# Kernel optimization log

Hardware: AMD Instinct MI355X
Metric: run time of the kernel (lower is better)

## Reference

```python
import jax, jax.numpy as jnp
import numpy as np

N_TOKENS = 262144
NUM_CODES = 512
CODE_DIM = 64


def setup_inputs() -> dict:
    key = jax.random.key(0)
    k1, k2 = jax.random.split(key)
    z_e = jax.random.normal(k1, (N_TOKENS, CODE_DIM), dtype=jnp.float32)
    embeddings = jax.random.normal(k2, (NUM_CODES, CODE_DIM), dtype=jnp.float32)
    return {"z_e": z_e, "embeddings": embeddings}


def reference(z_e, embeddings):
    # distances[n, k] = ||z_e[n] - e_k||^2, expanded matmul form as in the torch code
    # (N, K) = (N, 1) - 2 * (N, D) @ (D, K) + (K,)
    distances = (
        jnp.sum(z_e ** 2, axis=1, keepdims=True)
        - 2.0 * (z_e @ embeddings.T)
        + jnp.sum(embeddings ** 2, axis=1)
    )
    indices = jnp.argmin(distances, axis=1)          # (N,)
    z_q = embeddings[indices]                        # (N, D) gather
    # straight-through: identity gradient to z_e, none through the gather
    z_q_st = z_e + jax.lax.stop_gradient(z_q - z_e)
    commitment_loss = jnp.mean((jax.lax.stop_gradient(z_e) - z_q) ** 2)
    return z_q_st, indices, commitment_loss
```

## Files before the change

### kernel.cpp

```cpp
#include <hip/hip_runtime.h>


typedef short  bf16x8 __attribute__((ext_vector_type(8)));
typedef float  f32x4  __attribute__((ext_vector_type(4)));

static constexpr int N_TOK = 262144;
static constexpr int K     = 512;
static constexpr int D     = 64;
static constexpr float THRESH = 0.01f;
static constexpr int NBLK_A = N_TOK / 1024;

static constexpr size_t WS_ESQ   = 0;
static constexpr size_t WS_BL    = 2048;
static constexpr size_t WS_EFRAG = 10240;

#define GLDS16(G, L) __builtin_amdgcn_global_load_lds(                    \
    (const __attribute__((address_space(1))) void*)(G),                   \
    (__attribute__((address_space(3))) void*)(L), 16, 0, 0)

__global__ __launch_bounds__(512) void prep_kernel(
    const float* __restrict__ emb, unsigned short* __restrict__ ef,
    float* __restrict__ esq) {
  int idx  = blockIdx.x * 512 + threadIdx.x;
  int code = idx >> 6, d = idx & 63;
  float s  = -2.0f * emb[code * 64 + d];
  unsigned u  = __float_as_uint(s);
  unsigned hi = (u + 0x7FFFu + ((u >> 16) & 1u)) >> 16;
  float lof   = s - __uint_as_float(hi << 16);
  unsigned v2 = __float_as_uint(lof);
  unsigned lo = (v2 + 0x7FFFu + ((v2 >> 16) & 1u)) >> 16;
  int tile = code >> 4, row = code & 15;
  int c = (d >> 5) & 1, g = (d >> 3) & 3, i = d & 7;
  int lane = row + (g << 4);
  size_t base = ((size_t)tile * 256 + (size_t)c * 128) * 8;
  ef[base + (size_t)(0 * 64 + lane) * 8 + i] = (unsigned short)hi;
  ef[base + (size_t)(1 * 64 + lane) * 8 + i] = (unsigned short)lo;
  if (threadIdx.x < 8) {
    int k = blockIdx.x * 8 + threadIdx.x;
    const float4* row4 = reinterpret_cast<const float4*>(emb + (size_t)k * D);
    float acc = 0.f;
#pragma unroll
    for (int j = 0; j < 16; ++j) {
      float4 v = row4[j];
      acc = fmaf(v.x, v.x, acc); acc = fmaf(v.y, v.y, acc);
      acc = fmaf(v.z, v.z, acc); acc = fmaf(v.w, v.w, acc);
    }
    esq[k] = acc;
  }
}

__device__ __forceinline__ void split8(float4 a, float4 b,
                                       bf16x8& h, bf16x8& lo) {
  float v[8] = {a.x, a.y, a.z, a.w, b.x, b.y, b.z, b.w};
#pragma unroll
  for (int i = 0; i < 8; ++i) {
    unsigned u  = __float_as_uint(v[i]);
    unsigned hi = (u + 0x7FFFu + ((u >> 16) & 1u)) >> 16;
    float lof   = v[i] - __uint_as_float(hi << 16);
    unsigned v2 = __float_as_uint(lof);
    unsigned l2 = (v2 + 0x7FFFu + ((v2 >> 16) & 1u)) >> 16;
    h[i]  = (short)hi;
    lo[i] = (short)l2;
  }
}

#define ARGMIN4(C, BASE, BEST, SECOND, BIDXV)               \
  {                                                         \
    _Pragma("unroll")                                       \
    for (int r = 0; r < 4; ++r) {                           \
      float v = (C)[r];                                     \
      bool lt = v < (BEST);                                 \
      float mn = fminf((SECOND), v);                        \
      (SECOND) = lt ? (BEST) : mn;                          \
      (BIDXV)  = lt ? ((BASE) + r) : (BIDXV);               \
      (BEST)   = lt ? v : (BEST);                           \
    }                                                       \
  }

__global__ __launch_bounds__(1024) void vq_mfma(
    const float* __restrict__ z_e, const float* __restrict__ emb,
    const unsigned short* __restrict__ efrag, const float* __restrict__ esq_g,
    float* __restrict__ out_zq, float* __restrict__ out_idx,
    float* __restrict__ block_loss) {
  __shared__ float esql[K];
  __shared__ __align__(16) short lds_e[65536];
  __shared__ int   sIdx[512];
  __shared__ float wsm[16];

  const int t  = threadIdx.x;
  const int l  = t & 63;
  const int wu = __builtin_amdgcn_readfirstlane(t >> 6);
  const int g  = l >> 4, g4 = g << 2;
  const int blk0 = blockIdx.x * 1024;

  if (t < K) esql[t] = esq_g[t];

  const bf16x8* EF = reinterpret_cast<const bf16x8*>(efrag);
#pragma unroll
  for (int r = 0; r < 8; ++r)
    GLDS16(EF + r * 1024 + t, &lds_e[r * 8192 + wu * 512]);
  asm volatile("s_waitcnt vmcnt(0)" ::: "memory");
  __builtin_amdgcn_s_barrier();

  float blsum = 0.f;

  for (int pass = 0; pass < 2; ++pass) {
    const int tok0 = blk0 + pass * 512 + wu * 32;

    bf16x8 zh0A, zl0A, zh1A, zl1A, zh0B, zl0B, zh1B, zl1B;
    {
      const int rowA = tok0 + (l & 15);
      const float* zp = z_e + (size_t)rowA * D + g * 8;
      float4 q0 = *reinterpret_cast<const float4*>(zp);
      float4 q1 = *reinterpret_cast<const float4*>(zp + 4);
      float4 q2 = *reinterpret_cast<const float4*>(zp + 32);
      float4 q3 = *reinterpret_cast<const float4*>(zp + 36);
      split8(q0, q1, zh0A, zl0A);
      split8(q2, q3, zh1A, zl1A);
      zp += (size_t)16 * D;
      q0 = *reinterpret_cast<const float4*>(zp);
      q1 = *reinterpret_cast<const float4*>(zp + 4);
      q2 = *reinterpret_cast<const float4*>(zp + 32);
      q3 = *reinterpret_cast<const float4*>(zp + 36);
      split8(q0, q1, zh0B, zl0B);
      split8(q2, q3, zh1B, zl1B);
    }

    float bestA = 3.402823466e38f, secondA = 3.402823466e38f;
    float bestB = 3.402823466e38f, secondB = 3.402823466e38f;
    int idxA = 0, idxB = 0;

    for (int tile = 0; tile < 32; ++tile) {
      const bf16x8* tb =
          reinterpret_cast<const bf16x8*>(&lds_e[(size_t)tile * 2048]);
      f32x4 CA = *reinterpret_cast<const f32x4*>(&esql[tile * 16 + g4]);
      f32x4 CB = CA;
      bf16x8 e0h = tb[l], e0l = tb[64 + l];
      bf16x8 e1h = tb[128 + l], e1l = tb[192 + l];
      __builtin_amdgcn_s_setprio(1);
      CA = __builtin_amdgcn_mfma_f32_16x16x32_bf16(e0h, zh0A, CA, 0, 0, 0);
      CB = __builtin_amdgcn_mfma_f32_16x16x32_bf16(e0h, zh0B, CB, 0, 0, 0);
      CA = __builtin_amdgcn_mfma_f32_16x16x32_bf16(e0h, zl0A, CA, 0, 0, 0);
      CB = __builtin_amdgcn_mfma_f32_16x16x32_bf16(e0h, zl0B, CB, 0, 0, 0);
      CA = __builtin_amdgcn_mfma_f32_16x16x32_bf16(e0l, zh0A, CA, 0, 0, 0);
      CB = __builtin_amdgcn_mfma_f32_16x16x32_bf16(e0l, zh0B, CB, 0, 0, 0);
      CA = __builtin_amdgcn_mfma_f32_16x16x32_bf16(e1h, zh1A, CA, 0, 0, 0);
      CB = __builtin_amdgcn_mfma_f32_16x16x32_bf16(e1h, zh1B, CB, 0, 0, 0);
      CA = __builtin_amdgcn_mfma_f32_16x16x32_bf16(e1h, zl1A, CA, 0, 0, 0);
      CB = __builtin_amdgcn_mfma_f32_16x16x32_bf16(e1h, zl1B, CB, 0, 0, 0);
      CA = __builtin_amdgcn_mfma_f32_16x16x32_bf16(e1l, zh1A, CA, 0, 0, 0);
      CB = __builtin_amdgcn_mfma_f32_16x16x32_bf16(e1l, zh1B, CB, 0, 0, 0);
      __builtin_amdgcn_s_setprio(0);

      const int base = tile * 16 + g4;
      ARGMIN4(CA, base, bestA, secondA, idxA)
      ARGMIN4(CB, base, bestB, secondB, idxB)
    }

#pragma unroll
    for (int mask = 16; mask <= 32; mask <<= 1) {
      float ob, os; int oi; bool take; float hi2;
      ob = __shfl_xor(bestA, mask); oi = __shfl_xor(idxA, mask);
      os = __shfl_xor(secondA, mask);
      hi2 = fmaxf(bestA, ob);
      secondA = fminf(secondA, fminf(os, hi2));
      take = (ob < bestA) || (ob == bestA && oi < idxA);
      bestA = take ? ob : bestA; idxA = take ? oi : idxA;

      ob = __shfl_xor(bestB, mask); oi = __shfl_xor(idxB, mask);
      os = __shfl_xor(secondB, mask);
      hi2 = fmaxf(bestB, ob);
      secondB = fminf(secondB, fminf(os, hi2));
      take = (ob < bestB) || (ob == bestB && oi < idxB);
      bestB = take ? ob : bestB; idxB = take ? oi : idxB;
    }

    if (l < 16) {
      sIdx[wu * 32 + l]      = idxA;
      sIdx[wu * 32 + 16 + l] = idxB;
    }

    {
      bool fA = (l < 16) && ((secondA - bestA) < THRESH);
      bool fB = (l < 16) && ((secondB - bestB) < THRESH);
      unsigned long long ba = __ballot(fA);
      unsigned long long bb = __ballot(fB);
      unsigned mask = (unsigned)((ba & 0xFFFFull) | ((bb & 0xFFFFull) << 16));
      while (mask) {
        const int j = __builtin_ctz(mask);
        mask &= mask - 1;
        const int n = tok0 + j;
        const float4* zr =
            reinterpret_cast<const float4*>(z_e + (size_t)n * D);
        float best = 3.402823466e38f; int bid = 0;
#pragma unroll 1
        for (int half2 = 0; half2 < 2; ++half2) {
          float acc[4];
#pragma unroll
          for (int m = 0; m < 4; ++m) acc[m] = 0.f;
#pragma unroll 1
          for (int i = 0; i < 16; ++i) {
            float4 z4 = zr[i];
#pragma unroll
            for (int m = 0; m < 4; ++m) {
              const float4 e4 = *reinterpret_cast<const float4*>(
                  emb + (size_t)(l + 64 * (half2 * 4 + m)) * D + 4 * i);
              acc[m] = fmaf(z4.x, e4.x, acc[m]);
              acc[m] = fmaf(z4.y, e4.y, acc[m]);
              acc[m] = fmaf(z4.z, e4.z, acc[m]);
              acc[m] = fmaf(z4.w, e4.w, acc[m]);
            }
          }
#pragma unroll
          for (int m = 0; m < 4; ++m) {
            const int code = l + 64 * (half2 * 4 + m);
            float s = fmaf(-2.f, acc[m], esq_g[code]);
            if (s < best) { best = s; bid = code; }
          }
        }
#pragma unroll
        for (int mk = 1; mk <= 32; mk <<= 1) {
          float ob = __shfl_xor(best, mk);
          int   oi = __shfl_xor(bid, mk);
          bool take = (ob < best) || (ob == best && oi < bid);
          best = take ? ob : best;
          bid  = take ? oi : bid;
        }
        if (l == 0) sIdx[wu * 32 + j] = bid;
      }
    }

    {
      const int tk = l >> 1, h = l & 1;
      const int n = tok0 + tk;
      const int bi = sIdx[wu * 32 + tk];
      const float4* er =
          reinterpret_cast<const float4*>(emb + (size_t)bi * D);
      const float4* zr =
          reinterpret_cast<const float4*>(z_e + (size_t)n * D);
      float4* orow = reinterpret_cast<float4*>(out_zq + (size_t)n * D);
      float lsum = 0.f;
#pragma unroll
      for (int j = 0; j < 8; ++j) {
        int i = h * 8 + j;
        float4 Q = er[i], Z = zr[i];
        float dx = Q.x - Z.x, dy = Q.y - Z.y, dz = Q.z - Z.z, dw = Q.w - Z.w;
        float4 st;
        st.x = Z.x + dx; st.y = Z.y + dy; st.z = Z.z + dz; st.w = Z.w + dw;
        orow[i] = st;
        lsum = fmaf(dx, dx, lsum); lsum = fmaf(dy, dy, lsum);
        lsum = fmaf(dz, dz, lsum); lsum = fmaf(dw, dw, lsum);
      }
      if (h == 0) out_idx[n] = (float)bi;
      float s = lsum;
#pragma unroll
      for (int off = 32; off > 0; off >>= 1) s += __shfl_xor(s, off, 64);
      blsum += s;
    }
  }

  if (l == 0) wsm[wu] = blsum;
  __syncthreads();
  if (t == 0) {
    float s = 0.f;
#pragma unroll
    for (int i = 0; i < 16; ++i) s += wsm[i];
    block_loss[blockIdx.x] = s;
  }
}

__global__ __launch_bounds__(256) void loss_finalize(
    const float* __restrict__ bl, float* __restrict__ out_loss) {
  __shared__ float sm[256];
  const int t = threadIdx.x;
  sm[t] = bl[t];
  __syncthreads();
#pragma unroll
  for (int off = 128; off > 0; off >>= 1) {
    if (t < off) sm[t] += sm[t + off];
    __syncthreads();
  }
  if (t == 0) out_loss[0] = sm[0] * (1.0f / 16777216.0f);
}

extern "C" void kernel_launch(void* const* d_in, const int* in_sizes, int n_in,
                              void* d_out, int out_size, void* d_ws, size_t ws_size,
                              hipStream_t stream) {
  const float* z_e = (const float*)d_in[0];
  const float* emb = (const float*)d_in[1];

  float* out      = (float*)d_out;
  float* out_zq   = out;
  float* out_idx  = out + (size_t)N_TOK * D;
  float* out_loss = out_idx + N_TOK;

  char* wsb = (char*)d_ws;
  float*          esqp = (float*)(wsb + WS_ESQ);
  float*          bl   = (float*)(wsb + WS_BL);
  unsigned short* ef   = (unsigned short*)(wsb + WS_EFRAG);

  prep_kernel<<<64, 512, 0, stream>>>(emb, ef, esqp);
  vq_mfma<<<NBLK_A, 1024, 0, stream>>>(z_e, emb, ef, esqp, out_zq, out_idx, bl);
  loss_finalize<<<1, 256, 0, stream>>>(bl, out_loss);
}
```

Baseline: 104.0 us.

## Process 64 tokens per wave in one pass, overlapping z loads with LDS fill

Replaces the two-pass loop (32 tokens per wave per pass) with a single pass where each wave handles 64 tokens as four 16-row MFMA fragments. Each LDS codebook fragment load now feeds four MFMAs instead of two, and the z_e fragment loads are issued before the wait on the codebook LDS fill so the two overlap. The epilogue gives each lane one token row instead of pairing two lanes per row. This doubles accumulator and fragment register pressure, which may lower occupancy or cause spills, and the per-lane row stores are less coalesced.

Result: slower. 112.2 us (+7.8%).

```diff
diff --git a/kernel.cpp b/kernel.cpp
--- a/kernel.cpp
+++ b/kernel.cpp
@@ -77,6 +77,16 @@
     }                                                       \
   }
 
+#define ZFRAG(ZP, H0, L0, H1, L1)                                          \
+  {                                                                        \
+    float4 q0 = *reinterpret_cast<const float4*>(ZP);                      \
+    float4 q1 = *reinterpret_cast<const float4*>((ZP) + 4);                \
+    float4 q2 = *reinterpret_cast<const float4*>((ZP) + 32);               \
+    float4 q3 = *reinterpret_cast<const float4*>((ZP) + 36);               \
+    split8(q0, q1, H0, L0);                                                \
+    split8(q2, q3, H1, L1);                                                \
+  }
+
 __global__ __launch_bounds__(1024) void vq_mfma(
     const float* __restrict__ z_e, const float* __restrict__ emb,
     const unsigned short* __restrict__ efrag, const float* __restrict__ esq_g,
@@ -84,14 +94,14 @@
     float* __restrict__ block_loss) {
   __shared__ float esql[K];
   __shared__ __align__(16) short lds_e[65536];
-  __shared__ int   sIdx[512];
+  __shared__ int   sIdx[1024];
   __shared__ float wsm[16];
 
   const int t  = threadIdx.x;
   const int l  = t & 63;
   const int wu = __builtin_amdgcn_readfirstlane(t >> 6);
   const int g  = l >> 4, g4 = g << 2;
-  const int blk0 = blockIdx.x * 1024;
+  const int tok0 = blockIdx.x * 1024 + wu * 64;
 
   if (t < K) esql[t] = esq_g[t];
 
@@ -99,167 +109,175 @@
 #pragma unroll
   for (int r = 0; r < 8; ++r)
     GLDS16(EF + r * 1024 + t, &lds_e[r * 8192 + wu * 512]);
+
+  bf16x8 zh0A, zl0A, zh1A, zl1A, zh0B, zl0B, zh1B, zl1B;
+  bf16x8 zh0C, zl0C, zh1C, zl1C, zh0D, zl0D, zh1D, zl1D;
+  {
+    const float* zp = z_e + (size_t)(tok0 + (l & 15)) * D + g * 8;
+    ZFRAG(zp, zh0A, zl0A, zh1A, zl1A)
+    zp += (size_t)16 * D;
+    ZFRAG(zp, zh0B, zl0B, zh1B, zl1B)
+    zp += (size_t)16 * D;
+    ZFRAG(zp, zh0C, zl0C, zh1C, zl1C)
+    zp += (size_t)16 * D;
+    ZFRAG(zp, zh0D, zl0D, zh1D, zl1D)
+  }
+
   asm volatile("s_waitcnt vmcnt(0)" ::: "memory");
   __builtin_amdgcn_s_barrier();
 
-  float blsum = 0.f;
-
-  for (int pass = 0; pass < 2; ++pass) {
-    const int tok0 = blk0 + pass * 512 + wu * 32;
-
-    bf16x8 zh0A, zl0A, zh1A, zl1A, zh0B, zl0B, zh1B, zl1B;
+  float bestA = 3.402823466e38f, secondA = 3.402823466e38f;
+  float bestB = 3.402823466e38f, secondB = 3.402823466e38f;
+  float bestC = 3.402823466e38f, secondC = 3.402823466e38f;
+  float bestD = 3.402823466e38f, secondD = 3.402823466e38f;
+  int idxA = 0, idxB = 0, idxC = 0, idxD = 0;
+
+  for (int tile = 0; tile < 32; ++tile) {
+    const bf16x8* tb =
+        reinterpret_cast<const bf16x8*>(&lds_e[(size_t)tile * 2048]);
+    f32x4 CA = *reinterpret_cast<const f32x4*>(&esql[tile * 16 + g4]);
+    f32x4 CB = CA, CC = CA, CD = CA;
     {
-      const int rowA = tok0 + (l & 15);
-      const float* zp = z_e + (size_t)rowA * D + g * 8;
-      float4 q0 = *reinterpret_cast<const float4*>(zp);
-      float4 q1 = *reinterpret_cast<const float4*>(zp + 4);
-      float4 q2 = *reinterpret_cast<const float4*>(zp + 32);
-      float4 q3 = *reinterpret_cast<const float4*>(zp + 36);
-      split8(q0, q1, zh0A, zl0A);
-      split8(q2, q3, zh1A, zl1A);
-      zp += (size_t)16 * D;
-      q0 = *reinterpret_cast<const float4*>(zp);
-      q1 = *reinterpret_cast<const float4*>(zp + 4);
-      q2 = *reinterpret_cast<const float4*>(zp + 32);
-      q3 = *reinterpret_cast<const float4*>(zp + 36);
-      split8(q0, q1, zh0B, zl0B);
-      split8(q2, q3, zh1B, zl1B);
-    }
-
-    float bestA = 3.402823466e38f, secondA = 3.402823466e38f;
-    float bestB = 3.402823466e38f, secondB = 3.402823466e38f;
-    int idxA = 0, idxB = 0;
-
-    for (int tile = 0; tile < 32; ++tile) {
-      const bf16x8* tb =
-          reinterpret_cast<const bf16x8*>(&lds_e[(size_t)tile * 2048]);
-      f32x4 CA = *reinterpret_cast<const f32x4*>(&esql[tile * 16 + g4]);
-      f32x4 CB = CA;
       bf16x8 e0h = tb[l], e0l = tb[64 + l];
-      bf16x8 e1h = tb[128 + l], e1l = tb[192 + l];
       __builtin_amdgcn_s_setprio(1);
       CA = __builtin_amdgcn_mfma_f32_16x16x32_bf16(e0h, zh0A, CA, 0, 0, 0);
       CB = __builtin_amdgcn_mfma_f32_16x16x32_bf16(e0h, zh0B, CB, 0, 0, 0);
+      CC = __builtin_amdgcn_mfma_f32_16x16x32_bf16(e0h, zh0C, CC, 0, 0, 0);
+      CD = __builtin_amdgcn_mfma_f32_16x16x32_bf16(e0h, zh0D, CD, 0, 0, 0);
       CA = __builtin_amdgcn_mfma_f32_16x16x32_bf16(e0h, zl0A, CA, 0, 0, 0);
       CB = __builtin_amdgcn_mfma_f32_16x16x32_bf16(e0h, zl0B, CB, 0, 0, 0);
+      CC = __builtin_amdgcn_mfma_f32_16x16x32_bf16(e0h, zl0C, CC, 0, 0, 0);
+      CD = __builtin_amdgcn_mfma_f32_16x16x32_bf16(e0h, zl0D, CD, 0, 0, 0);
       CA = __builtin_amdgcn_mfma_f32_16x16x32_bf16(e0l, zh0A, CA, 0, 0, 0);
       CB = __builtin_amdgcn_mfma_f32_16x16x32_bf16(e0l, zh0B, CB, 0, 0, 0);
+      CC = __builtin_amdgcn_mfma_f32_16x16x32_bf16(e0l, zh0C, CC, 0, 0, 0);
+      CD = __builtin_amdgcn_mfma_f32_16x16x32_bf16(e0l, zh0D, CD, 0, 0, 0);
+      __builtin_amdgcn_s_setprio(0);
+    }
+    {
+      bf16x8 e1h = tb[128 + l], e1l = tb[192 + l];
+      __builtin_amdgcn_s_setprio(1);
       CA = __builtin_amdgcn_mfma_f32_16x16x32_bf16(e1h, zh1A, CA, 0, 0, 0);
       CB = __builtin_amdgcn_mfma_f32_16x16x32_bf16(e1h, zh1B, CB, 0, 0, 0);
+      CC = __builtin_amdgcn_mfma_f32_16x16x32_bf16(e1h, zh1C, CC, 0, 0, 0);
+      CD = __builtin_amdgcn_mfma_f32_16x16x32_bf16(e1h, zh1D, CD, 0, 0, 0);
       CA = __builtin_amdgcn_mfma_f32_16x16x32_bf16(e1h, zl1A, CA, 0, 0, 0);
       CB = __builtin_amdgcn_mfma_f32_16x16x32_bf16(e1h, zl1B, CB, 0, 0, 0);
+      CC = __builtin_amdgcn_mfma_f32_16x16x32_bf16(e1h, zl1C, CC, 0, 0, 0);
+      CD = __builtin_amdgcn_mfma_f32_16x16x32_bf16(e1h, zl1D, CD, 0, 0, 0);
       CA = __builtin_amdgcn_mfma_f32_16x16x32_bf16(e1l, zh1A, CA, 0, 0, 0);
       CB = __builtin_amdgcn_mfma_f32_16x16x32_bf16(e1l, zh1B, CB, 0, 0, 0);
+      CC = __builtin_amdgcn_mfma_f32_16x16x32_bf16(e1l, zh1C, CC, 0, 0, 0);
+      CD = __builtin_amdgcn_mfma_f32_16x16x32_bf16(e1l, zh1D, CD, 0, 0, 0);
       __builtin_amdgcn_s_setprio(0);
-
-      const int base = tile * 16 + g4;
-      ARGMIN4(CA, base, bestA, secondA, idxA)
-      ARGMIN4(CB, base, bestB, secondB, idxB)
-    }
-
-#pragma unroll
-    for (int mask = 16; mask <= 32; mask <<= 1) {
-      float ob, os; int oi; bool take; float hi2;
-      ob = __shfl_xor(bestA, mask); oi = __shfl_xor(idxA, mask);
-      os = __shfl_xor(secondA, mask);
-      hi2 = fmaxf(bestA, ob);
-      secondA = fminf(secondA, fminf(os, hi2));
-      take = (ob < bestA) || (ob == bestA && oi < idxA);
-      bestA = take ? ob : bestA; idxA = take ? oi : idxA;
-
-      ob = __shfl_xor(bestB, mask); oi = __shfl_xor(idxB, mask);
-      os = __shfl_xor(secondB, mask);
-      hi2 = fmaxf(bestB, ob);
-      secondB = fminf(secondB, fminf(os, hi2));
-      take = (ob < bestB) || (ob == bestB && oi < idxB);
-      bestB = take ? ob : bestB; idxB = take ? oi : idxB;
-    }
-
-    if (l < 16) {
-      sIdx[wu * 32 + l]      = idxA;
-      sIdx[wu * 32 + 16 + l] = idxB;
-    }
-
-    {
-      bool fA = (l < 16) && ((secondA - bestA) < THRESH);
-      bool fB = (l < 16) && ((secondB - bestB) < THRESH);
-      unsigned long long ba = __ballot(fA);
-      unsigned long long bb = __ballot(fB);
-      unsigned mask = (unsigned)((ba & 0xFFFFull) | ((bb & 0xFFFFull) << 16));
-      while (mask) {
-        const int j = __builtin_ctz(mask);
-        mask &= mask - 1;
-        const int n = tok0 + j;
-        const float4* zr =
-            reinterpret_cast<const float4*>(z_e + (size_t)n * D);
-        float best = 3.402823466e38f; int bid = 0;
+    }
+
+    const int base = tile * 16 + g4;
+    ARGMIN4(CA, base, bestA, secondA, idxA)
+    ARGMIN4(CB, base, bestB, secondB, idxB)
+    ARGMIN4(CC, base, bestC, secondC, idxC)
+    ARGMIN4(CD, base, bestD, secondD, idxD)
+  }
+
+#pragma unroll
+  for (int mask = 16; mask <= 32; mask <<= 1) {
+    float ob, os; int oi; bool take; float hi2;
+#define RED(BEST, SECOND, IDX)                                  \
+    ob = __shfl_xor(BEST, mask); oi = __shfl_xor(IDX, mask);    \
+    os = __shfl_xor(SECOND, mask);                              \
+    hi2 = fmaxf(BEST, ob);                                      \
+    SECOND = fminf(SECOND, fminf(os, hi2));                     \
+    take = (ob < BEST) || (ob == BEST && oi < IDX);             \
+    BEST = take ? ob : BEST; IDX = take ? oi : IDX;
+    RED(bestA, secondA, idxA)
+    RED(bestB, secondB, idxB)
+    RED(bestC, secondC, idxC)
+    RED(bestD, secondD, idxD)
+#undef RED
+  }
+
+  if (l < 16) {
+    sIdx[wu * 64 + l]      = idxA;
+    sIdx[wu * 64 + 16 + l] = idxB;
+    sIdx[wu * 64 + 32 + l] = idxC;
+    sIdx[wu * 64 + 48 + l] = idxD;
+  }
+
+  {
+    bool fA = (l < 16) && ((secondA - bestA) < THRESH);
+    bool fB = (l < 16) && ((secondB - bestB) < THRESH);
+    bool fC = (l < 16) && ((secondC - bestC) < THRESH);
+    bool fD = (l < 16) && ((secondD - bestD) < THRESH);
+    unsigned long long m =  (__ballot(fA) & 0xFFFFull)
+                         | ((__ballot(fB) & 0xFFFFull) << 16)
+                         | ((__ballot(fC) & 0xFFFFull) << 32)
+                         | ((__ballot(fD) & 0xFFFFull) << 48);
+    while (m) {
+      const int j = __builtin_ctzll(m);
+      m &= m - 1;
+      const int n = tok0 + j;
+      const float4* zr = reinterpret_cast<const float4*>(z_e + (size_t)n * D);
+      float best = 3.402823466e38f; int bid = 0;
 #pragma unroll 1
-        for (int half2 = 0; half2 < 2; ++half2) {
-          float acc[4];
-#pragma unroll
-          for (int m = 0; m < 4; ++m) acc[m] = 0.f;
+      for (int half2 = 0; half2 < 2; ++half2) {
+        float acc[4];
+#pragma unroll
+        for (int mm = 0; mm < 4; ++mm) acc[mm] = 0.f;
 #pragma unroll 1
-          for (int i = 0; i < 16; ++i) {
-            float4 z4 = zr[i];
-#pragma unroll
-            for (int m = 0; m < 4; ++m) {
-              const float4 e4 = *reinterpret_cast<const float4*>(
-                  emb + (size_t)(l + 64 * (half2 * 4 + m)) * D + 4 * i);
-              acc[m] = fmaf(z4.x, e4.x, acc[m]);
-              acc[m] = fmaf(z4.y, e4.y, acc[m]);
-              acc[m] = fmaf(z4.z, e4.z, acc[m]);
-              acc[m] = fmaf(z4.w, e4.w, acc[m]);
-            }
-          }
-#pragma unroll
-          for (int m = 0; m < 4; ++m) {
-            const int code = l + 64 * (half2 * 4 + m);
-            float s = fmaf(-2.f, acc[m], esq_g[code]);
-            if (s < best) { best = s; bid = code; }
+        for (int i = 0; i < 16; ++i) {
+          float4 z4 = zr[i];
+#pragma unroll
+          for (int mm = 0; mm < 4; ++mm) {
+            const float4 e4 = *reinterpret_cast<const float4*>(
+                emb + (size_t)(l + 64 * (half2 * 4 + mm)) * D + 4 * i);
+            acc[mm] = fmaf(z4.x, e4.x, acc[mm]);
+            acc[mm] = fmaf(z4.y, e4.y, acc[mm]);
+            acc[mm] = fmaf(z4.z, e4.z, acc[mm]);
+            acc[mm] = fmaf(z4.w, e4.w, acc[mm]);
           }
         }
 #pragma unroll
-        for (int mk = 1; mk <= 32; mk <<= 1) {
-          float ob = __shfl_xor(best, mk);
-          int   oi = __shfl_xor(bid, mk);
-          bool take = (ob < best) || (ob == best && oi < bid);
-          best = take ? ob : best;
-          bid  = take ? oi : bid;
+        for (int mm = 0; mm < 4; ++mm) {
+          const int code = l + 64 * (half2 * 4 + mm);
+          float s = fmaf(-2.f, acc[mm], esq_g[code]);
+          if (s < best) { best = s; bid = code; }
         }
-        if (l == 0) sIdx[wu * 32 + j] = bid;
       }
-    }
-
-    {
-      const int tk = l >> 1, h = l & 1;
-      const int n = tok0 + tk;
-      const int bi = sIdx[wu * 32 + tk];
-      const float4* er =
-          reinterpret_cast<const float4*>(emb + (size_t)bi * D);
-      const float4* zr =
-          reinterpret_cast<const float4*>(z_e + (size_t)n * D);
-      float4* orow = reinterpret_cast<float4*>(out_zq + (size_t)n * D);
-      float lsum = 0.f;
-#pragma unroll
-      for (int j = 0; j < 8; ++j) {
-        int i = h * 8 + j;
-        float4 Q = er[i], Z = zr[i];
-        float dx = Q.x - Z.x, dy = Q.y - Z.y, dz = Q.z - Z.z, dw = Q.w - Z.w;
-        float4 st;
-        st.x = Z.x + dx; st.y = Z.y + dy; st.z = Z.z + dz; st.w = Z.w + dw;
-        orow[i] = st;
-        lsum = fmaf(dx, dx, lsum); lsum = fmaf(dy, dy, lsum);
-        lsum = fmaf(dz, dz, lsum); lsum = fmaf(dw, dw, lsum);
+#pragma unroll
+      for (int mk = 1; mk <= 32; mk <<= 1) {
+        float ob = __shfl_xor(best, mk);
+        int   oi = __shfl_xor(bid, mk);
+        bool take = (ob < best) || (ob == best && oi < bid);
+        best = take ? ob : best;
+        bid  = take ? oi : bid;
       }
-      if (h == 0) out_idx[n] = (float)bi;
-      float s = lsum;
-#pragma unroll
-      for (int off = 32; off > 0; off >>= 1) s += __shfl_xor(s, off, 64);
-      blsum += s;
-    }
-  }
-
-  if (l == 0) wsm[wu] = blsum;
+      if (l == 0) sIdx[wu * 64 + j] = bid;
+    }
+  }
+
+  {
+    const int n = tok0 + l;
+    const int bi = sIdx[wu * 64 + l];
+    const float4* er = reinterpret_cast<const float4*>(emb + (size_t)bi * D);
+    const float4* zr = reinterpret_cast<const float4*>(z_e + (size_t)n * D);
+    float4* orow = reinterpret_cast<float4*>(out_zq + (size_t)n * D);
+    float lsum = 0.f;
+#pragma unroll 4
+    for (int i = 0; i < 16; ++i) {
+      float4 Q = er[i], Z = zr[i];
+      float dx = Q.x - Z.x, dy = Q.y - Z.y, dz = Q.z - Z.z, dw = Q.w - Z.w;
+      float4 st;
+      st.x = Z.x + dx; st.y = Z.y + dy; st.z = Z.z + dz; st.w = Z.w + dw;
+      orow[i] = st;
+      lsum = fmaf(dx, dx, lsum); lsum = fmaf(dy, dy, lsum);
+      lsum = fmaf(dz, dz, lsum); lsum = fmaf(dw, dw, lsum);
+    }
+    out_idx[n] = (float)bi;
+    float s = lsum;
+#pragma unroll
+    for (int off = 32; off > 0; off >>= 1) s += __shfl_xor(s, off, 64);
+    if (l == 0) wsm[wu] = s;
+  }
   __syncthreads();
   if (t == 0) {
     float s = 0.f;
```

## Stage only high-half codebook in LDS, read low half from global, one pass per block

Applied to the files above, without the earlier changes.

Halves the number of tokens per block (512 instead of 1024) so the grid doubles to 512 blocks, removing the two-pass loop. Only the high bf16 half of the codebook fragments is staged in LDS (64KB instead of 128KB), and the low half is read directly from global memory (L2/L1-cached) inside the tile loop. The z_e loads are issued before the LDS-staging wait so they overlap. The aim is lower LDS footprint and higher occupancy or more blocks per CU, at the cost of more codebook staging overall and global loads inside the hot MFMA loop. The loss finalize now sums 512 partials.

New measurement: 128.5 us. +23.6%, slower.

```diff
diff --git a/kernel.cpp b/kernel.cpp
--- a/kernel.cpp
+++ b/kernel.cpp
@@ -8,7 +8,7 @@
 static constexpr int K     = 512;
 static constexpr int D     = 64;
 static constexpr float THRESH = 0.01f;
-static constexpr int NBLK_A = N_TOK / 1024;
+static constexpr int NBLK_A = N_TOK / 512;
 
 static constexpr size_t WS_ESQ   = 0;
 static constexpr size_t WS_BL    = 2048;
@@ -83,7 +83,7 @@
     float* __restrict__ out_zq, float* __restrict__ out_idx,
     float* __restrict__ block_loss) {
   __shared__ float esql[K];
-  __shared__ __align__(16) short lds_e[65536];
+  __shared__ __align__(16) short lds_eh[32768];
   __shared__ int   sIdx[512];
   __shared__ float wsm[16];
 
@@ -91,175 +91,172 @@
   const int l  = t & 63;
   const int wu = __builtin_amdgcn_readfirstlane(t >> 6);
   const int g  = l >> 4, g4 = g << 2;
-  const int blk0 = blockIdx.x * 1024;
+  const int tok0 = blockIdx.x * 512 + wu * 32;
 
   if (t < K) esql[t] = esq_g[t];
 
   const bf16x8* EF = reinterpret_cast<const bf16x8*>(efrag);
 #pragma unroll
-  for (int r = 0; r < 8; ++r)
-    GLDS16(EF + r * 1024 + t, &lds_e[r * 8192 + wu * 512]);
+  for (int r = 0; r < 4; ++r) {
+    const int fh = r * 16 + wu;
+    const int tile = fh >> 1, c = fh & 1;
+    GLDS16(EF + (size_t)tile * 256 + c * 128 + l,
+           &lds_eh[r * 8192 + wu * 512]);
+  }
+
+  bf16x8 zh0A, zl0A, zh1A, zl1A, zh0B, zl0B, zh1B, zl1B;
+  {
+    const int rowA = tok0 + (l & 15);
+    const float* zp = z_e + (size_t)rowA * D + g * 8;
+    float4 q0 = *reinterpret_cast<const float4*>(zp);
+    float4 q1 = *reinterpret_cast<const float4*>(zp + 4);
+    float4 q2 = *reinterpret_cast<const float4*>(zp + 32);
+    float4 q3 = *reinterpret_cast<const float4*>(zp + 36);
+    split8(q0, q1, zh0A, zl0A);
+    split8(q2, q3, zh1A, zl1A);
+    zp += (size_t)16 * D;
+    q0 = *reinterpret_cast<const float4*>(zp);
+    q1 = *reinterpret_cast<const float4*>(zp + 4);
+    q2 = *reinterpret_cast<const float4*>(zp + 32);
+    q3 = *reinterpret_cast<const float4*>(zp + 36);
+    split8(q0, q1, zh0B, zl0B);
+    split8(q2, q3, zh1B, zl1B);
+  }
+
   asm volatile("s_waitcnt vmcnt(0)" ::: "memory");
   __builtin_amdgcn_s_barrier();
 
-  float blsum = 0.f;
-
-  for (int pass = 0; pass < 2; ++pass) {
-    const int tok0 = blk0 + pass * 512 + wu * 32;
-
-    bf16x8 zh0A, zl0A, zh1A, zl1A, zh0B, zl0B, zh1B, zl1B;
-    {
-      const int rowA = tok0 + (l & 15);
-      const float* zp = z_e + (size_t)rowA * D + g * 8;
-      float4 q0 = *reinterpret_cast<const float4*>(zp);
-      float4 q1 = *reinterpret_cast<const float4*>(zp + 4);
-      float4 q2 = *reinterpret_cast<const float4*>(zp + 32);
-      float4 q3 = *reinterpret_cast<const float4*>(zp + 36);
-      split8(q0, q1, zh0A, zl0A);
-      split8(q2, q3, zh1A, zl1A);
-      zp += (size_t)16 * D;
-      q0 = *reinterpret_cast<const float4*>(zp);
-      q1 = *reinterpret_cast<const float4*>(zp + 4);
-      q2 = *reinterpret_cast<const float4*>(zp + 32);
-      q3 = *reinterpret_cast<const float4*>(zp + 36);
-      split8(q0, q1, zh0B, zl0B);
-      split8(q2, q3, zh1B, zl1B);
-    }
-
-    float bestA = 3.402823466e38f, secondA = 3.402823466e38f;
-    float bestB = 3.402823466e38f, secondB = 3.402823466e38f;
-    int idxA = 0, idxB = 0;
-
-    for (int tile = 0; tile < 32; ++tile) {
-      const bf16x8* tb =
-          reinterpret_cast<const bf16x8*>(&lds_e[(size_t)tile * 2048]);
-      f32x4 CA = *reinterpret_cast<const f32x4*>(&esql[tile * 16 + g4]);
-      f32x4 CB = CA;
-      bf16x8 e0h = tb[l], e0l = tb[64 + l];
-      bf16x8 e1h = tb[128 + l], e1l = tb[192 + l];
-      __builtin_amdgcn_s_setprio(1);
-      CA = __builtin_amdgcn_mfma_f32_16x16x32_bf16(e0h, zh0A, CA, 0, 0, 0);
-      CB = __builtin_amdgcn_mfma_f32_16x16x32_bf16(e0h, zh0B, CB, 0, 0, 0);
-      CA = __builtin_amdgcn_mfma_f32_16x16x32_bf16(e0h, zl0A, CA, 0, 0, 0);
-      CB = __builtin_amdgcn_mfma_f32_16x16x32_bf16(e0h, zl0B, CB, 0, 0, 0);
-      CA = __builtin_amdgcn_mfma_f32_16x16x32_bf16(e0l, zh0A, CA, 0, 0, 0);
-      CB = __builtin_amdgcn_mfma_f32_16x16x32_bf16(e0l, zh0B, CB, 0, 0, 0);
-      CA = __builtin_amdgcn_mfma_f32_16x16x32_bf16(e1h, zh1A, CA, 0, 0, 0);
-      CB = __builtin_amdgcn_mfma_f32_16x16x32_bf16(e1h, zh1B, CB, 0, 0, 0);
-      CA = __builtin_amdgcn_mfma_f32_16x16x32_bf16(e1h, zl1A, CA, 0, 0, 0);
-      CB = __builtin_amdgcn_mfma_f32_16x16x32_bf16(e1h, zl1B, CB, 0, 0, 0);
-      CA = __builtin_amdgcn_mfma_f32_16x16x32_bf16(e1l, zh1A, CA, 0, 0, 0);
-      CB = __builtin_amdgcn_mfma_f32_16x16x32_bf16(e1l, zh1B, CB, 0, 0, 0);
-      __builtin_amdgcn_s_setprio(0);
-
-      const int base = tile * 16 + g4;
-      ARGMIN4(CA, base, bestA, secondA, idxA)
-      ARGMIN4(CB, base, bestB, secondB, idxB)
-    }
-
-#pragma unroll
-    for (int mask = 16; mask <= 32; mask <<= 1) {
-      float ob, os; int oi; bool take; float hi2;
-      ob = __shfl_xor(bestA, mask); oi = __shfl_xor(idxA, mask);
-      os = __shfl_xor(secondA, mask);
-      hi2 = fmaxf(bestA, ob);
-      secondA = fminf(secondA, fminf(os, hi2));
-      take = (ob < bestA) || (ob == bestA && oi < idxA);
-      bestA = take ? ob : bestA; idxA = take ? oi : idxA;
-
-      ob = __shfl_xor(bestB, mask); oi = __shfl_xor(idxB, mask);
-      os = __shfl_xor(secondB, mask);
-      hi2 = fmaxf(bestB, ob);
-      secondB = fminf(secondB, fminf(os, hi2));
-      take = (ob < bestB) || (ob == bestB && oi < idxB);
-      bestB = take ? ob : bestB; idxB = take ? oi : idxB;
-    }
-
-    if (l < 16) {
-      sIdx[wu * 32 + l]      = idxA;
-      sIdx[wu * 32 + 16 + l] = idxB;
-    }
-
-    {
-      bool fA = (l < 16) && ((secondA - bestA) < THRESH);
-      bool fB = (l < 16) && ((secondB - bestB) < THRESH);
-      unsigned long long ba = __ballot(fA);
-      unsigned long long bb = __ballot(fB);
-      unsigned mask = (unsigned)((ba & 0xFFFFull) | ((bb & 0xFFFFull) << 16));
-      while (mask) {
-        const int j = __builtin_ctz(mask);
-        mask &= mask - 1;
-        const int n = tok0 + j;
-        const float4* zr =
-            reinterpret_cast<const float4*>(z_e + (size_t)n * D);
-        float best = 3.402823466e38f; int bid = 0;
+  float bestA = 3.402823466e38f, secondA = 3.402823466e38f;
+  float bestB = 3.402823466e38f, secondB = 3.402823466e38f;
+  int idxA = 0, idxB = 0;
+
+  for (int tile = 0; tile < 32; ++tile) {
+    const bf16x8* loP = EF + (size_t)tile * 256 + 64 + l;
+    bf16x8 e0l = loP[0];
+    bf16x8 e1l = loP[128];
+    const bf16x8* tbh =
+        reinterpret_cast<const bf16x8*>(&lds_eh[(size_t)tile * 1024]);
+    bf16x8 e0h = tbh[l], e1h = tbh[64 + l];
+
+    f32x4 CA = *reinterpret_cast<const f32x4*>(&esql[tile * 16 + g4]);
+    f32x4 CB = CA;
+    __builtin_amdgcn_s_setprio(1);
+    CA = __builtin_amdgcn_mfma_f32_16x16x32_bf16(e0h, zh0A, CA, 0, 0, 0);
+    CB = __builtin_amdgcn_mfma_f32_16x16x32_bf16(e0h, zh0B, CB, 0, 0, 0);
+    CA = __builtin_amdgcn_mfma_f32_16x16x32_bf16(e0h, zl0A, CA, 0, 0, 0);
+    CB = __builtin_amdgcn_mfma_f32_16x16x32_bf16(e0h, zl0B, CB, 0, 0, 0);
+    CA = __builtin_amdgcn_mfma_f32_16x16x32_bf16(e0l, zh0A, CA, 0, 0, 0);
+    CB = __builtin_amdgcn_mfma_f32_16x16x32_bf16(e0l, zh0B, CB, 0, 0, 0);
+    CA = __builtin_amdgcn_mfma_f32_16x16x32_bf16(e1h, zh1A, CA, 0, 0, 0);
+    CB = __builtin_amdgcn_mfma_f32_16x16x32_bf16(e1h, zh1B, CB, 0, 0, 0);
+    CA = __builtin_amdgcn_mfma_f32_16x16x32_bf16(e1h, zl1A, CA, 0, 0, 0);
+    CB = __builtin_amdgcn_mfma_f32_16x16x32_bf16(e1h, zl1B, CB, 0, 0, 0);
+    CA = __builtin_amdgcn_mfma_f32_16x16x32_bf16(e1l, zh1A, CA, 0, 0, 0);
+    CB = __builtin_amdgcn_mfma_f32_16x16x32_bf16(e1l, zh1B, CB, 0, 0, 0);
+    __builtin_amdgcn_s_setprio(0);
+
+    const int base = tile * 16 + g4;
+    ARGMIN4(CA, base, bestA, secondA, idxA)
+    ARGMIN4(CB, base, bestB, secondB, idxB)
+  }
+
+#pragma unroll
+  for (int mask = 16; mask <= 32; mask <<= 1) {
+    float ob, os; int oi; bool take; float hi2;
+    ob = __shfl_xor(bestA, mask); oi = __shfl_xor(idxA, mask);
+    os = __shfl_xor(secondA, mask);
+    hi2 = fmaxf(bestA, ob);
+    secondA = fminf(secondA, fminf(os, hi2));
+    take = (ob < bestA) || (ob == bestA && oi < idxA);
+    bestA = take ? ob : bestA; idxA = take ? oi : idxA;
+
+    ob = __shfl_xor(bestB, mask); oi = __shfl_xor(idxB, mask);
+    os = __shfl_xor(secondB, mask);
+    hi2 = fmaxf(bestB, ob);
+    secondB = fminf(secondB, fminf(os, hi2));
+    take = (ob < bestB) || (ob == bestB && oi < idxB);
+    bestB = take ? ob : bestB; idxB = take ? oi : idxB;
+  }
+
+  if (l < 16) {
+    sIdx[wu * 32 + l]      = idxA;
+    sIdx[wu * 32 + 16 + l] = idxB;
+  }
+
+  {
+    bool fA = (l < 16) && ((secondA - bestA) < THRESH);
+    bool fB = (l < 16) && ((secondB - bestB) < THRESH);
+    unsigned long long ba = __ballot(fA);
+    unsigned long long bb = __ballot(fB);
+    unsigned mask = (unsigned)((ba & 0xFFFFull) | ((bb & 0xFFFFull) << 16));
+    while (mask) {
+      const int j = __builtin_ctz(mask);
+      mask &= mask - 1;
+      const int n = tok0 + j;
+      const float4* zr = reinterpret_cast<const float4*>(z_e + (size_t)n * D);
+      float best = 3.402823466e38f; int bid = 0;
 #pragma unroll 1
-        for (int half2 = 0; half2 < 2; ++half2) {
-          float acc[4];
-#pragma unroll
-          for (int m = 0; m < 4; ++m) acc[m] = 0.f;
+      for (int half2 = 0; half2 < 2; ++half2) {
+        float acc[4];
+#pragma unroll
+        for (int m = 0; m < 4; ++m) acc[m] = 0.f;
 #pragma unroll 1
-          for (int i = 0; i < 16; ++i) {
-            float4 z4 = zr[i];
-#pragma unroll
-            for (int m = 0; m < 4; ++m) {
-              const float4 e4 = *reinterpret_cast<const float4*>(
-                  emb + (size_t)(l + 64 * (half2 * 4 + m)) * D + 4 * i);
-              acc[m] = fmaf(z4.x, e4.x, acc[m]);
-              acc[m] = fmaf(z4.y, e4.y, acc[m]);
-              acc[m] = fmaf(z4.z, e4.z, acc[m]);
-              acc[m] = fmaf(z4.w, e4.w, acc[m]);
-            }
-          }
+        for (int i = 0; i < 16; ++i) {
+          float4 z4 = zr[i];
 #pragma unroll
           for (int m = 0; m < 4; ++m) {
-            const int code = l + 64 * (half2 * 4 + m);
-            float s = fmaf(-2.f, acc[m], esq_g[code]);
-            if (s < best) { best = s; bid = code; }
+            const float4 e4 = *reinterpret_cast<const float4*>(
+                emb + (size_t)(l + 64 * (half2 * 4 + m)) * D + 4 * i);
+            acc[m] = fmaf(z4.x, e4.x, acc[m]);
+            acc[m] = fmaf(z4.y, e4.y, acc[m]);
+            acc[m] = fmaf(z4.z, e4.z, acc[m]);
+            acc[m] = fmaf(z4.w, e4.w, acc[m]);
           }
         }
 #pragma unroll
-        for (int mk = 1; mk <= 32; mk <<= 1) {
-          float ob = __shfl_xor(best, mk);
-          int   oi = __shfl_xor(bid, mk);
-          bool take = (ob < best) || (ob == best && oi < bid);
-          best = take ? ob : best;
-          bid  = take ? oi : bid;
+        for (int m = 0; m < 4; ++m) {
+          const int code = l + 64 * (half2 * 4 + m);
+          float s = fmaf(-2.f, acc[m], esq_g[code]);
+          if (s < best) { best = s; bid = code; }
         }
-        if (l == 0) sIdx[wu * 32 + j] = bid;
       }
+#pragma unroll
+      for (int mk = 1; mk <= 32; mk <<= 1) {
+        float ob = __shfl_xor(best, mk);
+        int   oi = __shfl_xor(bid, mk);
+        bool take = (ob < best) || (ob == best && oi < bid);
+        best = take ? ob : best;
+        bid  = take ? oi : bid;
+      }
+      if (l == 0) sIdx[wu * 32 + j] = bid;
     }
-
-    {
-      const int tk = l >> 1, h = l & 1;
-      const int n = tok0 + tk;
-      const int bi = sIdx[wu * 32 + tk];
-      const float4* er =
-          reinterpret_cast<const float4*>(emb + (size_t)bi * D);
-      const float4* zr =
-          reinterpret_cast<const float4*>(z_e + (size_t)n * D);
-      float4* orow = reinterpret_cast<float4*>(out_zq + (size_t)n * D);
-      float lsum = 0.f;
-#pragma unroll
-      for (int j = 0; j < 8; ++j) {
-        int i = h * 8 + j;
-        float4 Q = er[i], Z = zr[i];
-        float dx = Q.x - Z.x, dy = Q.y - Z.y, dz = Q.z - Z.z, dw = Q.w - Z.w;
-        float4 st;
-        st.x = Z.x + dx; st.y = Z.y + dy; st.z = Z.z + dz; st.w = Z.w + dw;
-        orow[i] = st;
-        lsum = fmaf(dx, dx, lsum); lsum = fmaf(dy, dy, lsum);
-        lsum = fmaf(dz, dz, lsum); lsum = fmaf(dw, dw, lsum);
-      }
-      if (h == 0) out_idx[n] = (float)bi;
-      float s = lsum;
-#pragma unroll
-      for (int off = 32; off > 0; off >>= 1) s += __shfl_xor(s, off, 64);
-      blsum += s;
+  }
+
+  {
+    const int tk = l >> 1, h = l & 1;
+    const int n = tok0 + tk;
+    const int bi = sIdx[wu * 32 + tk];
+    const float4* er = reinterpret_cast<const float4*>(emb + (size_t)bi * D);
+    const float4* zr = reinterpret_cast<const float4*>(z_e + (size_t)n * D);
+    float4* orow = reinterpret_cast<float4*>(out_zq + (size_t)n * D);
+    float lsum = 0.f;
+#pragma unroll
+    for (int j = 0; j < 8; ++j) {
+      int i = h * 8 + j;
+      float4 Q = er[i], Z = zr[i];
+      float dx = Q.x - Z.x, dy = Q.y - Z.y, dz = Q.z - Z.z, dw = Q.w - Z.w;
+      float4 st;
+      st.x = Z.x + dx; st.y = Z.y + dy; st.z = Z.z + dz; st.w = Z.w + dw;
+      orow[i] = st;
+      lsum = fmaf(dx, dx, lsum); lsum = fmaf(dy, dy, lsum);
+      lsum = fmaf(dz, dz, lsum); lsum = fmaf(dw, dw, lsum);
     }
-  }
-
-  if (l == 0) wsm[wu] = blsum;
+    if (h == 0) out_idx[n] = (float)bi;
+    float s = lsum;
+#pragma unroll
+    for (int off = 32; off > 0; off >>= 1) s += __shfl_xor(s, off, 64);
+    if (l == 0) wsm[wu] = s;
+  }
   __syncthreads();
   if (t == 0) {
     float s = 0.f;
@@ -273,7 +270,7 @@
     const float* __restrict__ bl, float* __restrict__ out_loss) {
   __shared__ float sm[256];
   const int t = threadIdx.x;
-  sm[t] = bl[t];
+  sm[t] = bl[t] + bl[t + 256];
   __syncthreads();
 #pragma unroll
   for (int off = 128; off > 0; off >>= 1) {
```
